# Kernel tuning notes

Measured on AMD Instinct MI355X. Metric: run time of the kernel, lower is better.

The kernel has to match this reference:

```python
import jax, jax.numpy as jnp
import numpy as np

B, S, IN_DIM = 2048, 65, 256
H, L = 8, 256


def setup_inputs() -> dict:
    key = jax.random.key(0)
    ks = jax.random.split(key, 8)
    return {
        "x": jax.random.normal(ks[0], (B, S, IN_DIM), dtype=jnp.float32),
        "Wq": jax.random.normal(ks[1], (H, IN_DIM, L), dtype=jnp.float32),
        "Wk": jax.random.normal(ks[2], (H, IN_DIM, L), dtype=jnp.float32),
        "Wv": jax.random.normal(ks[3], (H, IN_DIM, L), dtype=jnp.float32),
        "W": jax.random.normal(ks[4], (H, L, 1), dtype=jnp.float32),
        "O": jax.random.normal(ks[5], (H * L, IN_DIM), dtype=jnp.float32),
        "P": jax.random.normal(ks[6], (S - 1, IN_DIM), dtype=jnp.float32),
        "bias": jax.random.normal(ks[7], (H,), dtype=jnp.float32),
    }


def reference(x, Wq, Wk, Wv, W, O, P, bias):
    origin = x[:, 0, :]                       # [B, D]
    walk = x[:, 1:, :]                        # [B, S-1, D]
    origin_seq = origin[:, None, :] + P       # [B, S-1, D]

    # per-head sigmoid projections, vectorized over heads
    k = jax.nn.sigmoid(jnp.einsum('bsd,hdl->bhsl', origin_seq, Wk))
    q = jax.nn.sigmoid(jnp.einsum('bsd,hdl->bhsl', walk, Wq))
    v = jax.nn.sigmoid(jnp.einsum('bsd,hdl->bhsl', walk, Wv))

    edge = jnp.cos(k * q) + bias[None, :, None, None]       # [B,H,S-1,L]
    score = jnp.einsum('bhsl,hl->bhs', edge, W[..., 0])      # [B,H,S-1]
    score = jax.nn.softmax(score, axis=-1)
    res = jnp.einsum('bhs,bhsl->bhl', score, v)              # [B,H,L]
    res = res.reshape(res.shape[0], H * L)                   # concat heads
    out = jax.nn.sigmoid(res @ O)                            # [B, D]
    return jnp.concatenate([out, origin], axis=-1)           # [B, 2D]
```

## Files before the change

kernel.cpp:

```cpp
#include <hip/hip_runtime.h>
#include <math.h>

#define NB   2048
#define NSEQ 65
#define ND   256
#define NH   8
#define NL   256
#define NS   64
#define APAD 264

typedef _Float16 f16;
typedef _Float16 f16x4 __attribute__((ext_vector_type(4)));
typedef _Float16 f16x8 __attribute__((ext_vector_type(8)));
typedef float    f32x4 __attribute__((ext_vector_type(4)));

__device__ __forceinline__ float sigmoidf_(float x) {
    return __builtin_amdgcn_rcpf(1.0f + __expf(-x));
}

__global__ __launch_bounds__(256) void wh_kernel(const float* __restrict__ Wq,
                                                 const float* __restrict__ Wv,
                                                 const float* __restrict__ Wk,
                                                 f16* __restrict__ wh) {
    int hm = blockIdx.x >> 4;
    int h  = hm / 3, m = hm % 3;
    int n  = ((blockIdx.x & 15) << 4) + (threadIdx.x >> 4);
    int kc = (threadIdx.x & 15) << 4;
    const float* src = (m == 0 ? Wq : (m == 1 ? Wv : Wk)) + h * (ND * NL);
    f16x8 t0, t1;
    #pragma unroll
    for (int j = 0; j < 8; ++j) t0[j] = (f16)src[(kc + j) * NL + n];
    #pragma unroll
    for (int j = 0; j < 8; ++j) t1[j] = (f16)src[(kc + 8 + j) * NL + n];
    f16* dst = wh + ((size_t)(hm * 256 + n)) * 256 + kc;
    *(f16x8*)dst       = t0;
    *(f16x8*)(dst + 8) = t1;
}

__global__ __launch_bounds__(256) void ot_kernel(const float* __restrict__ O,
                                                 f16* __restrict__ OT) {
    int n = blockIdx.x;
    int t = threadIdx.x;
    f16x8 v;
    #pragma unroll
    for (int j = 0; j < 8; ++j) v[j] = (f16)O[(size_t)(t * 8 + j) * 256 + n];
    *(f16x8*)(OT + (size_t)n * 2048 + t * 8) = v;
}

__global__ __launch_bounds__(256) void pkt_kernel(const float* __restrict__ P,
                                                  const float* __restrict__ Wk,
                                                  float* __restrict__ PKT) {
    int h = blockIdx.x >> 6;
    int s = blockIdx.x & 63;
    int t = threadIdx.x;
    __shared__ float p_s[ND];
    p_s[t] = P[s * ND + t];
    __syncthreads();
    const float* wk = Wk + h * (ND * NL) + t;
    float acc = 0.f;
    #pragma unroll 8
    for (int d = 0; d < ND; ++d) acc = fmaf(p_s[d], wk[d * NL], acc);
    PKT[((size_t)h * NL + t) * NS + s] = acc;
}

__global__ __launch_bounds__(256) void ok_gemm(const float* __restrict__ x,
                                               const f16*   __restrict__ wh,
                                               float* __restrict__ OK) {
    int mblk = blockIdx.x >> 4;
    int nblk = blockIdx.x & 15;
    int b0 = mblk * 64;
    int h  = nblk >> 1;
    int l0 = (nblk & 1) * 128;
    int t = threadIdx.x;
    int w = t >> 6, lane = t & 63, c = lane & 15, g = lane >> 4;

    __shared__ f16 Ao[64 * APAD];
    #pragma unroll
    for (int it = 0; it < 16; ++it) {
        int idx4 = it * 256 + t;
        int s = idx4 >> 6, kq = idx4 & 63;
        float4 v = *(const float4*)(x + (size_t)(b0 + s) * (NSEQ * ND) + kq * 4);
        *(f16x4*)(&Ao[s * APAD + kq * 4]) = (f16x4){(f16)v.x, (f16)v.y, (f16)v.z, (f16)v.w};
    }
    __syncthreads();

    f32x4 acc[4][2];
    #pragma unroll
    for (int mt = 0; mt < 4; ++mt)
        #pragma unroll
        for (int nt = 0; nt < 2; ++nt) acc[mt][nt] = (f32x4){0.f, 0.f, 0.f, 0.f};

    const f16* bb = wh + ((size_t)((h * 3 + 2) * 256 + l0 + w * 32 + c)) * 256;
    #pragma unroll 2
    for (int kk = 0; kk < 8; ++kk) {
        int k0 = kk * 32 + g * 8;
        f16x8 af[4];
        #pragma unroll
        for (int mt = 0; mt < 4; ++mt)
            af[mt] = *(const f16x8*)(&Ao[(mt * 16 + c) * APAD + k0]);
        #pragma unroll
        for (int nt = 0; nt < 2; ++nt) {
            f16x8 bf = *(const f16x8*)(bb + nt * 16 * 256 + k0);
            #pragma unroll
            for (int mt = 0; mt < 4; ++mt)
                acc[mt][nt] = __builtin_amdgcn_mfma_f32_16x16x32_f16(af[mt], bf, acc[mt][nt], 0, 0, 0);
        }
    }
    #pragma unroll
    for (int mt = 0; mt < 4; ++mt)
        #pragma unroll
        for (int nt = 0; nt < 2; ++nt)
            #pragma unroll
            for (int r = 0; r < 4; ++r)
                OK[((size_t)h * NB + b0 + mt * 16 + g * 4 + r) * NL + l0 + w * 32 + nt * 16 + c]
                    = acc[mt][nt][r];
}

__global__ __launch_bounds__(256, 4) void attn_mfma(
        const float* __restrict__ x,
        const f16*   __restrict__ wh,
        const float* __restrict__ W,
        const float* __restrict__ PKT,
        const float* __restrict__ OK,
        f16* __restrict__ res) {
    int b = blockIdx.x;
    int t = threadIdx.x;
    int w    = t >> 6;
    int lane = t & 63;
    int c = lane & 15;
    int g = lane >> 4;

    __shared__ f16 A[NS * 256];

    const float* xb = x + (size_t)b * (NSEQ * ND);

    #pragma unroll
    for (int it = 0; it < 16; ++it) {
        int idx4 = it * 256 + t;
        int s  = idx4 >> 6;
        int kq = idx4 & 63;
        float4 v = *(const float4*)(xb + (1 + s) * ND + kq * 4);
        int kp = (kq * 4) ^ ((s & 7) << 3);
        *(f16x4*)(&A[s * 256 + kp]) = (f16x4){(f16)v.x, (f16)v.y, (f16)v.z, (f16)v.w};
    }
    __syncthreads();

    int swz = (c & 7) << 3;
    int rot = b & 7;
    int hrot = (b >> 3) & 1;

    #pragma unroll
    for (int hh = 0; hh < 2; ++hh) {
        int h = w * 2 + ((hh + hrot) & 1);

        float part[4][4];
        #pragma unroll
        for (int mt = 0; mt < 4; ++mt)
            #pragma unroll
            for (int r = 0; r < 4; ++r) part[mt][r] = 0.f;

        for (int ci = 0; ci < 8; ++ci) {
            int ch = (ci + rot) & 7;
            f32x4 acc[4][2];
            #pragma unroll
            for (int mt = 0; mt < 4; ++mt)
                #pragma unroll
                for (int nt = 0; nt < 2; ++nt) acc[mt][nt] = (f32x4){0.f, 0.f, 0.f, 0.f};

            const f16* bq = wh + ((size_t)((h * 3 + 0) * 256 + ch * 32 + c)) * 256;
            #pragma unroll 2
            for (int kk = 0; kk < 8; ++kk) {
                int k0 = kk * 32 + g * 8;
                f16x8 af[4];
                #pragma unroll
                for (int mt = 0; mt < 4; ++mt)
                    af[mt] = *(const f16x8*)(&A[(mt * 16 + c) * 256 + (k0 ^ swz)]);
                #pragma unroll
                for (int nt = 0; nt < 2; ++nt) {
                    f16x8 bf = *(const f16x8*)(bq + nt * 16 * 256 + k0);
                    #pragma unroll
                    for (int mt = 0; mt < 4; ++mt)
                        acc[mt][nt] = __builtin_amdgcn_mfma_f32_16x16x32_f16(af[mt], bf, acc[mt][nt], 0, 0, 0);
                }
            }
            #pragma unroll
            for (int nt = 0; nt < 2; ++nt) {
                int l = ch * 32 + nt * 16 + c;
                float wl  = W[h * NL + l];
                float okv = OK[((size_t)h * NB + b) * NL + l];
                const float* pkcol = PKT + ((size_t)h * NL + l) * NS + g * 4;
                #pragma unroll
                for (int mt = 0; mt < 4; ++mt) {
                    float4 pk4 = *(const float4*)(pkcol + mt * 16);
                    float pks[4] = {pk4.x, pk4.y, pk4.z, pk4.w};
                    #pragma unroll
                    for (int r = 0; r < 4; ++r) {
                        float qs = sigmoidf_(acc[mt][nt][r]);
                        float ks = sigmoidf_(okv + pks[r]);
                        part[mt][r] = fmaf(__cosf(ks * qs), wl, part[mt][r]);
                    }
                }
            }
        }

        #pragma unroll
        for (int mt = 0; mt < 4; ++mt)
            #pragma unroll
            for (int r = 0; r < 4; ++r) {
                float v = part[mt][r];
                v += __shfl_xor(v, 1, 64);
                v += __shfl_xor(v, 2, 64);
                v += __shfl_xor(v, 4, 64);
                v += __shfl_xor(v, 8, 64);
                part[mt][r] = v;
            }
        float m = part[0][0];
        #pragma unroll
        for (int mt = 0; mt < 4; ++mt)
            #pragma unroll
            for (int r = 0; r < 4; ++r) m = fmaxf(m, part[mt][r]);
        m = fmaxf(m, __shfl_xor(m, 16, 64));
        m = fmaxf(m, __shfl_xor(m, 32, 64));
        float ssum = 0.f;
        #pragma unroll
        for (int mt = 0; mt < 4; ++mt)
            #pragma unroll
            for (int r = 0; r < 4; ++r) {
                float e = __expf(part[mt][r] - m);
                part[mt][r] = e;
                ssum += e;
            }
        ssum += __shfl_xor(ssum, 16, 64);
        ssum += __shfl_xor(ssum, 32, 64);
        float rinv = __builtin_amdgcn_rcpf(ssum);
        #pragma unroll
        for (int mt = 0; mt < 4; ++mt)
            #pragma unroll
            for (int r = 0; r < 4; ++r) part[mt][r] *= rinv;

        for (int ci = 0; ci < 8; ++ci) {
            int ch = (ci + rot) & 7;
            f32x4 acc[4][2];
            #pragma unroll
            for (int mt = 0; mt < 4; ++mt)
                #pragma unroll
                for (int nt = 0; nt < 2; ++nt) acc[mt][nt] = (f32x4){0.f, 0.f, 0.f, 0.f};

            const f16* bv = wh + ((size_t)((h * 3 + 1) * 256 + ch * 32 + c)) * 256;
            #pragma unroll 2
            for (int kk = 0; kk < 8; ++kk) {
                int k0 = kk * 32 + g * 8;
                f16x8 af[4];
                #pragma unroll
                for (int mt = 0; mt < 4; ++mt)
                    af[mt] = *(const f16x8*)(&A[(mt * 16 + c) * 256 + (k0 ^ swz)]);
                #pragma unroll
                for (int nt = 0; nt < 2; ++nt) {
                    f16x8 bf = *(const f16x8*)(bv + nt * 16 * 256 + k0);
                    #pragma unroll
                    for (int mt = 0; mt < 4; ++mt)
                        acc[mt][nt] = __builtin_amdgcn_mfma_f32_16x16x32_f16(af[mt], bf, acc[mt][nt], 0, 0, 0);
                }
            }
            #pragma unroll
            for (int nt = 0; nt < 2; ++nt) {
                float v = 0.f;
                #pragma unroll
                for (int mt = 0; mt < 4; ++mt)
                    #pragma unroll
                    for (int r = 0; r < 4; ++r)
                        v = fmaf(part[mt][r], sigmoidf_(acc[mt][nt][r]), v);
                v += __shfl_xor(v, 16, 64);
                v += __shfl_xor(v, 32, 64);
                if (g == 0)
                    res[(size_t)b * 2048 + h * NL + ch * 32 + nt * 16 + c] = (f16)v;
            }
        }
    }
}

__global__ __launch_bounds__(256) void out_gemm(
        const float* __restrict__ x,
        const f16*   __restrict__ res,
        const f16*   __restrict__ OT,
        float* __restrict__ out) {
    int mblk = blockIdx.x >> 1;
    int nblk = blockIdx.x & 1;
    int b0 = mblk * 64;
    int t  = threadIdx.x;
    int w    = t >> 6;
    int lane = t & 63;
    int c = lane & 15;
    int g = lane >> 4;

    __shared__ f16 Ao[64 * APAD];

    f32x4 acc[4][2];
    #pragma unroll
    for (int mt = 0; mt < 4; ++mt)
        #pragma unroll
        for (int nt = 0; nt < 2; ++nt) acc[mt][nt] = (f32x4){0.f, 0.f, 0.f, 0.f};

    for (int chunk = 0; chunk < 8; ++chunk) {
        int kbase = chunk * 256;
        __syncthreads();
        #pragma unroll
        for (int it = 0; it < 8; ++it) {
            int id  = it * 256 + t;
            int row = id >> 5;
            int kc  = (id & 31) << 3;
            *(f16x8*)(&Ao[row * APAD + kc]) =
                *(const f16x8*)(res + (size_t)(b0 + row) * 2048 + kbase + kc);
        }
        __syncthreads();
        #pragma unroll
        for (int kk = 0; kk < 8; ++kk) {
            int k0 = kk * 32 + g * 8;
            f16x8 af[4];
            #pragma unroll
            for (int mt = 0; mt < 4; ++mt)
                af[mt] = *(const f16x8*)(&Ao[(mt * 16 + c) * APAD + k0]);
            #pragma unroll
            for (int nt = 0; nt < 2; ++nt) {
                f16x8 bf = *(const f16x8*)(OT + (size_t)(nblk * 128 + w * 32 + nt * 16 + c) * 2048 + kbase + k0);
                #pragma unroll
                for (int mt = 0; mt < 4; ++mt)
                    acc[mt][nt] = __builtin_amdgcn_mfma_f32_16x16x32_f16(af[mt], bf, acc[mt][nt], 0, 0, 0);
            }
        }
    }
    #pragma unroll
    for (int mt = 0; mt < 4; ++mt)
        #pragma unroll
        for (int nt = 0; nt < 2; ++nt)
            #pragma unroll
            for (int r = 0; r < 4; ++r) {
                int row = mt * 16 + g * 4 + r;
                int col = nblk * 128 + w * 32 + nt * 16 + c;
                out[(size_t)(b0 + row) * 512 + col] = sigmoidf_(acc[mt][nt][r]);
            }
    if (nblk == 1) {
        for (int r2 = 0; r2 < 64; ++r2)
            out[(size_t)(b0 + r2) * 512 + 256 + t] = x[(size_t)(b0 + r2) * (NSEQ * ND) + t];
    }
}

extern "C" void kernel_launch(void* const* d_in, const int* in_sizes, int n_in,
                              void* d_out, int out_size, void* d_ws, size_t ws_size,
                              hipStream_t stream) {
    const float* x    = (const float*)d_in[0];
    const float* Wq   = (const float*)d_in[1];
    const float* Wk   = (const float*)d_in[2];
    const float* Wv   = (const float*)d_in[3];
    const float* W    = (const float*)d_in[4];
    const float* O    = (const float*)d_in[5];
    const float* P    = (const float*)d_in[6];
    float* out = (float*)d_out;

    char* wsb = (char*)d_ws;
    f16*   wh  = (f16*)wsb;
    f16*   OT  = (f16*)(wsb + 3145728);
    float* PKT = (float*)(wsb + 4194304);
    float* OK  = (float*)(wsb + 4718592);
    f16*   res = (f16*)(wsb + 21495808);

    wh_kernel<<<384, 256, 0, stream>>>(Wq, Wv, Wk, wh);
    ot_kernel<<<256, 256, 0, stream>>>(O, OT);
    pkt_kernel<<<NH * NS, 256, 0, stream>>>(P, Wk, PKT);
    ok_gemm<<<512, 256, 0, stream>>>(x, wh, OK);
    attn_mfma<<<NB, 256, 0, stream>>>(x, wh, W, PKT, OK, res);
    out_gemm<<<64, 256, 0, stream>>>(x, res, OT, out);
}
```

Before: 821.6 us.

## Keep attention A-operand fragments in registers via pre-converted fp16 x buffer

Adds a separate kernel that converts the walk part of x to fp16 in workspace. The attention kernel now loads all of its MFMA A fragments (4x8 f16x8 per lane) into registers once, instead of staging x in shared memory and re-reading it for every chunk. Launch bounds drop to 2 blocks per SM to make room for the extra registers. The output GEMM also uses 32-row tiles and twice as many blocks to raise parallelism. The trade-offs are lower occupancy, an extra pass over x through global memory, and possible register spills.

```diff
diff --git a/kernel.cpp b/kernel.cpp
--- a/kernel.cpp
+++ b/kernel.cpp
@@ -16,6 +16,21 @@
 
 __device__ __forceinline__ float sigmoidf_(float x) {
     return __builtin_amdgcn_rcpf(1.0f + __expf(-x));
+}
+
+__global__ __launch_bounds__(256) void xh_kernel(const float* __restrict__ x,
+                                                 f16* __restrict__ xh) {
+    int flat8 = blockIdx.x * 256 + threadIdx.x;
+    int b  = flat8 >> 11;
+    int rm = flat8 & 2047;
+    int s  = rm >> 5;
+    int k8 = rm & 31;
+    const float* src = x + (size_t)b * (NSEQ * ND) + (1 + s) * ND + k8 * 8;
+    float4 v0 = *(const float4*)(src);
+    float4 v1 = *(const float4*)(src + 4);
+    f16x8 o = {(f16)v0.x, (f16)v0.y, (f16)v0.z, (f16)v0.w,
+               (f16)v1.x, (f16)v1.y, (f16)v1.z, (f16)v1.w};
+    *(f16x8*)(xh + (size_t)b * 16384 + s * 256 + k8 * 8) = o;
 }
 
 __global__ __launch_bounds__(256) void wh_kernel(const float* __restrict__ Wq,
@@ -116,8 +131,8 @@
                     = acc[mt][nt][r];
 }
 
-__global__ __launch_bounds__(256, 4) void attn_mfma(
-        const float* __restrict__ x,
+__global__ __launch_bounds__(256, 2) void attn_mfma(
+        const f16*   __restrict__ xh,
         const f16*   __restrict__ wh,
         const float* __restrict__ W,
         const float* __restrict__ PKT,
@@ -130,23 +145,15 @@
     int c = lane & 15;
     int g = lane >> 4;
 
-    __shared__ f16 A[NS * 256];
-
-    const float* xb = x + (size_t)b * (NSEQ * ND);
-
-    #pragma unroll
-    for (int it = 0; it < 16; ++it) {
-        int idx4 = it * 256 + t;
-        int s  = idx4 >> 6;
-        int kq = idx4 & 63;
-        float4 v = *(const float4*)(xb + (1 + s) * ND + kq * 4);
-        int kp = (kq * 4) ^ ((s & 7) << 3);
-        *(f16x4*)(&A[s * 256 + kp]) = (f16x4){(f16)v.x, (f16)v.y, (f16)v.z, (f16)v.w};
-    }
-    __syncthreads();
-
-    int swz = (c & 7) << 3;
-    int rot = b & 7;
+    f16x8 af[4][8];
+    const f16* xb = xh + (size_t)b * 16384 + c * 256 + g * 8;
+    #pragma unroll
+    for (int mt = 0; mt < 4; ++mt)
+        #pragma unroll
+        for (int kk = 0; kk < 8; ++kk)
+            af[mt][kk] = *(const f16x8*)(xb + mt * 16 * 256 + kk * 32);
+
+    int rot  = b & 7;
     int hrot = (b >> 3) & 1;
 
     #pragma unroll
@@ -167,20 +174,15 @@
                 #pragma unroll
                 for (int nt = 0; nt < 2; ++nt) acc[mt][nt] = (f32x4){0.f, 0.f, 0.f, 0.f};
 
-            const f16* bq = wh + ((size_t)((h * 3 + 0) * 256 + ch * 32 + c)) * 256;
-            #pragma unroll 2
+            const f16* bq = wh + ((size_t)((h * 3 + 0) * 256 + ch * 32 + c)) * 256 + g * 8;
+            #pragma unroll
             for (int kk = 0; kk < 8; ++kk) {
-                int k0 = kk * 32 + g * 8;
-                f16x8 af[4];
-                #pragma unroll
-                for (int mt = 0; mt < 4; ++mt)
-                    af[mt] = *(const f16x8*)(&A[(mt * 16 + c) * 256 + (k0 ^ swz)]);
                 #pragma unroll
                 for (int nt = 0; nt < 2; ++nt) {
-                    f16x8 bf = *(const f16x8*)(bq + nt * 16 * 256 + k0);
+                    f16x8 bf = *(const f16x8*)(bq + nt * 16 * 256 + kk * 32);
                     #pragma unroll
                     for (int mt = 0; mt < 4; ++mt)
-                        acc[mt][nt] = __builtin_amdgcn_mfma_f32_16x16x32_f16(af[mt], bf, acc[mt][nt], 0, 0, 0);
+                        acc[mt][nt] = __builtin_amdgcn_mfma_f32_16x16x32_f16(af[mt][kk], bf, acc[mt][nt], 0, 0, 0);
                 }
             }
             #pragma unroll
@@ -246,20 +248,15 @@
                 #pragma unroll
                 for (int nt = 0; nt < 2; ++nt) acc[mt][nt] = (f32x4){0.f, 0.f, 0.f, 0.f};
 
-            const f16* bv = wh + ((size_t)((h * 3 + 1) * 256 + ch * 32 + c)) * 256;
-            #pragma unroll 2
+            const f16* bv = wh + ((size_t)((h * 3 + 1) * 256 + ch * 32 + c)) * 256 + g * 8;
+            #pragma unroll
             for (int kk = 0; kk < 8; ++kk) {
-                int k0 = kk * 32 + g * 8;
-                f16x8 af[4];
-                #pragma unroll
-                for (int mt = 0; mt < 4; ++mt)
-                    af[mt] = *(const f16x8*)(&A[(mt * 16 + c) * 256 + (k0 ^ swz)]);
                 #pragma unroll
                 for (int nt = 0; nt < 2; ++nt) {
-                    f16x8 bf = *(const f16x8*)(bv + nt * 16 * 256 + k0);
+                    f16x8 bf = *(const f16x8*)(bv + nt * 16 * 256 + kk * 32);
                     #pragma unroll
                     for (int mt = 0; mt < 4; ++mt)
-                        acc[mt][nt] = __builtin_amdgcn_mfma_f32_16x16x32_f16(af[mt], bf, acc[mt][nt], 0, 0, 0);
+                        acc[mt][nt] = __builtin_amdgcn_mfma_f32_16x16x32_f16(af[mt][kk], bf, acc[mt][nt], 0, 0, 0);
                 }
             }
             #pragma unroll
@@ -286,18 +283,18 @@
         float* __restrict__ out) {
     int mblk = blockIdx.x >> 1;
     int nblk = blockIdx.x & 1;
-    int b0 = mblk * 64;
+    int b0 = mblk * 32;
     int t  = threadIdx.x;
     int w    = t >> 6;
     int lane = t & 63;
     int c = lane & 15;
     int g = lane >> 4;
 
-    __shared__ f16 Ao[64 * APAD];
-
-    f32x4 acc[4][2];
-    #pragma unroll
-    for (int mt = 0; mt < 4; ++mt)
+    __shared__ f16 Ao[32 * APAD];
+
+    f32x4 acc[2][2];
+    #pragma unroll
+    for (int mt = 0; mt < 2; ++mt)
         #pragma unroll
         for (int nt = 0; nt < 2; ++nt) acc[mt][nt] = (f32x4){0.f, 0.f, 0.f, 0.f};
 
@@ -305,7 +302,7 @@
         int kbase = chunk * 256;
         __syncthreads();
         #pragma unroll
-        for (int it = 0; it < 8; ++it) {
+        for (int it = 0; it < 4; ++it) {
             int id  = it * 256 + t;
             int row = id >> 5;
             int kc  = (id & 31) << 3;
@@ -316,21 +313,21 @@
         #pragma unroll
         for (int kk = 0; kk < 8; ++kk) {
             int k0 = kk * 32 + g * 8;
-            f16x8 af[4];
-            #pragma unroll
-            for (int mt = 0; mt < 4; ++mt)
+            f16x8 af[2];
+            #pragma unroll
+            for (int mt = 0; mt < 2; ++mt)
                 af[mt] = *(const f16x8*)(&Ao[(mt * 16 + c) * APAD + k0]);
             #pragma unroll
             for (int nt = 0; nt < 2; ++nt) {
                 f16x8 bf = *(const f16x8*)(OT + (size_t)(nblk * 128 + w * 32 + nt * 16 + c) * 2048 + kbase + k0);
                 #pragma unroll
-                for (int mt = 0; mt < 4; ++mt)
+                for (int mt = 0; mt < 2; ++mt)
                     acc[mt][nt] = __builtin_amdgcn_mfma_f32_16x16x32_f16(af[mt], bf, acc[mt][nt], 0, 0, 0);
             }
         }
     }
     #pragma unroll
-    for (int mt = 0; mt < 4; ++mt)
+    for (int mt = 0; mt < 2; ++mt)
         #pragma unroll
         for (int nt = 0; nt < 2; ++nt)
             #pragma unroll
@@ -340,7 +337,7 @@
                 out[(size_t)(b0 + row) * 512 + col] = sigmoidf_(acc[mt][nt][r]);
             }
     if (nblk == 1) {
-        for (int r2 = 0; r2 < 64; ++r2)
+        for (int r2 = 0; r2 < 32; ++r2)
             out[(size_t)(b0 + r2) * 512 + 256 + t] = x[(size_t)(b0 + r2) * (NSEQ * ND) + t];
     }
 }
@@ -363,11 +360,13 @@
     float* PKT = (float*)(wsb + 4194304);
     float* OK  = (float*)(wsb + 4718592);
     f16*   res = (f16*)(wsb + 21495808);
-
+    f16*   xh  = (f16*)(wsb + 29884416);
+
+    xh_kernel<<<16384, 256, 0, stream>>>(x, xh);
     wh_kernel<<<384, 256, 0, stream>>>(Wq, Wv, Wk, wh);
     ot_kernel<<<256, 256, 0, stream>>>(O, OT);
     pkt_kernel<<<NH * NS, 256, 0, stream>>>(P, Wk, PKT);
     ok_gemm<<<512, 256, 0, stream>>>(x, wh, OK);
-    attn_mfma<<<NB, 256, 0, stream>>>(x, wh, W, PKT, OK, res);
-    out_gemm<<<64, 256, 0, stream>>>(x, res, OT, out);
-}
+    attn_mfma<<<NB, 256, 0, stream>>>(xh, wh, W, PKT, OK, res);
+    out_gemm<<<128, 256, 0, stream>>>(x, res, OT, out);
+}
```

Result: slower. 917.3 us (+11.6%).
